# Kernel optimization log

Measured on AMD Instinct MI355X. Metric: run time of the kernel, lower is better.

## Reference

```python
import jax, jax.numpy as jnp
import numpy as np

SEQ_LEN = 256
INPUT_DIM = 1
HIDDEN = 1024
CLASSES = 10
BATCH = 256


def _uniform_param(key, shape, fan):
    # matches torch _parameter: uniform(-1/sqrt(y), 1/sqrt(y)), y = shape[1] if rank>1 else 1
    stdv = 1.0 / np.sqrt(fan)
    return jax.random.uniform(key, shape, jnp.float32, -stdv, stdv)


def setup_inputs() -> dict:
    key = jax.random.key(0)
    k0, k1, k2, k3, k4, k5 = jax.random.split(key, 6)
    x = jax.random.normal(k0, (BATCH, SEQ_LEN), jnp.float32)
    return {
        "x": x,
        "W_hx": _uniform_param(k1, (INPUT_DIM, HIDDEN), HIDDEN),
        "W_hh": _uniform_param(k2, (HIDDEN, HIDDEN), HIDDEN),
        "W_ph": _uniform_param(k3, (HIDDEN, CLASSES), CLASSES),
        "b_h": _uniform_param(k4, (HIDDEN,), 1),
        "b_p": _uniform_param(k5, (CLASSES,), 1),
    }


def reference(x, W_hx, W_hh, W_ph, b_h, b_p):
    # With INPUT_DIM == 1, x[:, t:t+1] is just column t; build [seq, batch, 1] for scan.
    xs = jnp.swapaxes(x, 0, 1)[:, :, None]  # [S, B, 1]
    h0 = jnp.zeros((x.shape[0], HIDDEN), x.dtype)

    def step(h_prev, x_t):
        h_t = jnp.tanh(x_t @ W_hx + h_prev @ W_hh + b_h)  # [B, H]
        return h_t, None

    h_last, _ = jax.lax.scan(step, h0, xs)
    # Original computes p_t each step but only returns the last; compute only the last.
    return h_last @ W_ph + b_p  # [B, C]
```

## Files before the change

### kernel.cpp

```cpp
#include <hip/hip_runtime.h>
#include <stdint.h>

#define SEQ   256
#define BATCH 256
#define HID   1024
#define NCLS  10

#define NWG     128
#define THREADS 512
#define PLANEB  (32 * 16 * 64 * 16)

typedef __attribute__((ext_vector_type(8))) short bf16x8;
typedef __attribute__((ext_vector_type(4))) float f32x4;
typedef __attribute__((ext_vector_type(4))) unsigned int u32x4;

__device__ __forceinline__ unsigned short f2bf(float f) {
  unsigned u = __builtin_bit_cast(unsigned, f);
  u = (u + 0x7FFFu + ((u >> 16) & 1u)) >> 16;
  return (unsigned short)u;
}
__device__ __forceinline__ float bf2f(unsigned short h) {
  unsigned u = ((unsigned)h) << 16;
  return __builtin_bit_cast(float, u);
}
__device__ __forceinline__ float fast_tanh(float x) {
  float ax = __builtin_fabsf(x);
  float e = __expf(2.0f * ax);
  float t = 1.0f - 2.0f / (e + 1.0f);
  return __builtin_copysignf(t, x);
}
__device__ __forceinline__ unsigned tag_of(unsigned t) {
  return ((t >> 1) & 1u) ^ 1u;
}

__global__ __launch_bounds__(THREADS, 2) void rnn_asmpoll(
    const float* __restrict__ x, const float* __restrict__ Whx,
    const float* __restrict__ Whh, const float* __restrict__ Wph,
    const float* __restrict__ bh, const float* __restrict__ bp,
    float* __restrict__ out, unsigned char* __restrict__ ws)
{
  __shared__ f32x4 red[8][7][64];
  __shared__ unsigned long long pkbuf[8][64];

  const int tid  = threadIdx.x;
  const int lane = tid & 63;
  const int wv   = tid >> 6;
  const int l15  = lane & 15;
  const int q    = lane >> 4;

  const int gb = blockIdx.x >> 4;
  const int s  = blockIdx.x & 15;

  unsigned char* p0 = ws;
  unsigned char* p1 = ws + PLANEB;

  bf16x8 whi[4][4], wlo[4][4];
#pragma unroll
  for (int i = 0; i < 4; ++i) {
    const int ks = wv * 4 + i;
#pragma unroll
    for (int rt = 0; rt < 4; ++rt) {
      const int n = s * 64 + rt * 16 + l15;
#pragma unroll
      for (int j = 0; j < 8; ++j) {
        int k = ks * 32 + 4 * q + (j & 3) + 16 * (j >> 2);
        float w = Whh[(size_t)k * HID + n];
        unsigned short hi = f2bf(w);
        whi[i][rt][j] = (short)hi;
        wlo[i][rt][j] = (short)f2bf(w - bf2f(hi));
      }
    }
  }

  const int rt_o = wv >> 1, bt_o = wv & 1;
  const int b_own = gb * 32 + bt_o * 16 + l15;
  const float* xrow = x + (size_t)b_own * SEQ;
  const float4 whx4 = *(const float4*)(Whx + s * 64 + rt_o * 16 + q * 4);
  const float4 bh4  = *(const float4*)(bh  + s * 64 + rt_o * 16 + q * 4);
  const size_t soff = ((size_t)((s * 2 + (wv >> 2)) * 16 + gb * 2 + (wv & 1)) * 64 + lane) * 16;
  volatile u32x4* st0 = (volatile u32x4*)(p0 + soff);
  volatile u32x4* st1 = (volatile u32x4*)(p1 + soff);

  const size_t oA0 = ((size_t)((wv * 4 + 0) * 16 + gb * 2) * 64 + lane) * 16;
  const size_t oA1 = ((size_t)((wv * 4 + 1) * 16 + gb * 2) * 64 + lane) * 16;
  const size_t oA2 = ((size_t)((wv * 4 + 2) * 16 + gb * 2) * 64 + lane) * 16;
  const size_t oA3 = ((size_t)((wv * 4 + 3) * 16 + gb * 2) * 64 + lane) * 16;

  for (int t = 0; t < SEQ; ++t) {
    const unsigned tauW = tag_of((unsigned)t);
    const float xb = xrow[t];

    f32x4 acc[4][2];
#pragma unroll
    for (int rt = 0; rt < 4; ++rt)
#pragma unroll
      for (int bt = 0; bt < 2; ++bt) acc[rt][bt] = (f32x4){0.f, 0.f, 0.f, 0.f};

    if (t > 0) {
      const unsigned tauR = tag_of((unsigned)(t - 1));
      const unsigned char* rp = (t & 1) ? p0 : p1;
      const unsigned char* b0 = rp + oA0;
      const unsigned char* b1 = rp + oA1;
      const unsigned char* b2 = rp + oA2;
      const unsigned char* b3 = rp + oA3;
      u32x4 f0, f1, f2, f3, f4, f5, f6, f7;

      for (;;) {
        unsigned s0, s1, s2, s3, s4, s5, s6, s7;
        asm volatile(
          "global_load_dword %0, %8, off sc0 sc1\n\t"
          "global_load_dword %1, %8, off offset:1024 sc0 sc1\n\t"
          "global_load_dword %2, %9, off sc0 sc1\n\t"
          "global_load_dword %3, %9, off offset:1024 sc0 sc1\n\t"
          "global_load_dword %4, %10, off sc0 sc1\n\t"
          "global_load_dword %5, %10, off offset:1024 sc0 sc1\n\t"
          "global_load_dword %6, %11, off sc0 sc1\n\t"
          "global_load_dword %7, %11, off offset:1024 sc0 sc1\n\t"
          "s_waitcnt vmcnt(0)"
          : "=&v"(s0), "=&v"(s1), "=&v"(s2), "=&v"(s3),
            "=&v"(s4), "=&v"(s5), "=&v"(s6), "=&v"(s7)
          : "v"(b0), "v"(b1), "v"(b2), "v"(b3)
          : "memory");
        __builtin_amdgcn_sched_barrier(0);
        unsigned bad = ((s0 ^ tauR) | (s1 ^ tauR) | (s2 ^ tauR) | (s3 ^ tauR) |
                        (s4 ^ tauR) | (s5 ^ tauR) | (s6 ^ tauR) | (s7 ^ tauR)) & 1u;
        if (!__all((int)(bad == 0))) { __builtin_amdgcn_s_sleep(1); continue; }

        asm volatile(
          "global_load_dwordx4 %0, %8, off sc0 sc1\n\t"
          "global_load_dwordx4 %1, %8, off offset:1024 sc0 sc1\n\t"
          "global_load_dwordx4 %2, %9, off sc0 sc1\n\t"
          "global_load_dwordx4 %3, %9, off offset:1024 sc0 sc1\n\t"
          "global_load_dwordx4 %4, %10, off sc0 sc1\n\t"
          "global_load_dwordx4 %5, %10, off offset:1024 sc0 sc1\n\t"
          "global_load_dwordx4 %6, %11, off sc0 sc1\n\t"
          "global_load_dwordx4 %7, %11, off offset:1024 sc0 sc1\n\t"
          "s_waitcnt vmcnt(0)"
          : "=&v"(f0), "=&v"(f1), "=&v"(f2), "=&v"(f3),
            "=&v"(f4), "=&v"(f5), "=&v"(f6), "=&v"(f7)
          : "v"(b0), "v"(b1), "v"(b2), "v"(b3)
          : "memory");
        __builtin_amdgcn_sched_barrier(0);
        unsigned vb = ((f0[0] ^ tauR) | (f0[1] ^ tauR) | (f0[2] ^ tauR) | (f0[3] ^ tauR) |
                       (f1[0] ^ tauR) | (f1[1] ^ tauR) | (f1[2] ^ tauR) | (f1[3] ^ tauR) |
                       (f2[0] ^ tauR) | (f2[1] ^ tauR) | (f2[2] ^ tauR) | (f2[3] ^ tauR) |
                       (f3[0] ^ tauR) | (f3[1] ^ tauR) | (f3[2] ^ tauR) | (f3[3] ^ tauR) |
                       (f4[0] ^ tauR) | (f4[1] ^ tauR) | (f4[2] ^ tauR) | (f4[3] ^ tauR) |
                       (f5[0] ^ tauR) | (f5[1] ^ tauR) | (f5[2] ^ tauR) | (f5[3] ^ tauR) |
                       (f6[0] ^ tauR) | (f6[1] ^ tauR) | (f6[2] ^ tauR) | (f6[3] ^ tauR) |
                       (f7[0] ^ tauR) | (f7[1] ^ tauR) | (f7[2] ^ tauR) | (f7[3] ^ tauR)) & 1u;
        if (__all((int)(vb == 0))) break;
        __builtin_amdgcn_s_sleep(1);
      }

#define MSTEP(F, I, BT)                                                        \
      { bf16x8 a_ = __builtin_bit_cast(bf16x8, F);                             \
        acc[0][BT] = __builtin_amdgcn_mfma_f32_16x16x32_bf16(whi[I][0], a_, acc[0][BT], 0, 0, 0); \
        acc[0][BT] = __builtin_amdgcn_mfma_f32_16x16x32_bf16(wlo[I][0], a_, acc[0][BT], 0, 0, 0); \
        acc[1][BT] = __builtin_amdgcn_mfma_f32_16x16x32_bf16(whi[I][1], a_, acc[1][BT], 0, 0, 0); \
        acc[1][BT] = __builtin_amdgcn_mfma_f32_16x16x32_bf16(wlo[I][1], a_, acc[1][BT], 0, 0, 0); \
        acc[2][BT] = __builtin_amdgcn_mfma_f32_16x16x32_bf16(whi[I][2], a_, acc[2][BT], 0, 0, 0); \
        acc[2][BT] = __builtin_amdgcn_mfma_f32_16x16x32_bf16(wlo[I][2], a_, acc[2][BT], 0, 0, 0); \
        acc[3][BT] = __builtin_amdgcn_mfma_f32_16x16x32_bf16(whi[I][3], a_, acc[3][BT], 0, 0, 0); \
        acc[3][BT] = __builtin_amdgcn_mfma_f32_16x16x32_bf16(wlo[I][3], a_, acc[3][BT], 0, 0, 0); }
      MSTEP(f0, 0, 0) MSTEP(f1, 0, 1) MSTEP(f2, 1, 0) MSTEP(f3, 1, 1)
      MSTEP(f4, 2, 0) MSTEP(f5, 2, 1) MSTEP(f6, 3, 0) MSTEP(f7, 3, 1)
#undef MSTEP
    }

#pragma unroll
    for (int T = 0; T < 8; ++T)
      if (T != wv)
        red[T][(wv > T) ? (wv - 1) : wv][lane] = acc[T >> 1][T & 1];
    __syncthreads();

    f32x4 ssum = acc[rt_o][bt_o];
#pragma unroll
    for (int pr = 0; pr < 7; ++pr) ssum += red[wv][pr][lane];

    const float v0 = fast_tanh(ssum[0] + xb * whx4.x + bh4.x);
    const float v1 = fast_tanh(ssum[1] + xb * whx4.y + bh4.y);
    const float v2 = fast_tanh(ssum[2] + xb * whx4.z + bh4.z);
    const float v3 = fast_tanh(ssum[3] + xb * whx4.w + bh4.w);
    unsigned w0 = ((unsigned)f2bf(v0) | ((unsigned)f2bf(v1) << 16));
    unsigned w1 = ((unsigned)f2bf(v2) | ((unsigned)f2bf(v3) << 16));
    w0 = (w0 & ~1u) | tauW;
    w1 = (w1 & ~1u) | tauW;
    unsigned long long pk = (unsigned long long)w0 | ((unsigned long long)w1 << 32);
    pkbuf[wv][lane] = pk;
    __syncthreads();

    if (!(wv & 2)) {
      unsigned long long pk2 = pkbuf[wv | 2][lane];
      u32x4 st;
      st[0] = (unsigned)pk;  st[1] = (unsigned)(pk >> 32);
      st[2] = (unsigned)pk2; st[3] = (unsigned)(pk2 >> 32);
      if (t & 1) *st1 = st; else *st0 = st;
    }
  }

  if (s != 0) return;
  {
    const unsigned tauF = tag_of(255u);
    u32x4 hf[4][2];
    for (;;) {
#pragma unroll
      for (int i = 0; i < 4; ++i)
#pragma unroll
        for (int bt = 0; bt < 2; ++bt)
          hf[i][bt] = *(const volatile u32x4*)
              (p1 + ((size_t)((wv * 4 + i) * 16 + gb * 2 + bt) * 64 + lane) * 16);
      unsigned bad = 0;
#pragma unroll
      for (int i = 0; i < 4; ++i)
#pragma unroll
        for (int bt = 0; bt < 2; ++bt)
#pragma unroll
          for (int w = 0; w < 4; ++w) bad |= (hf[i][bt][w] ^ tauF) & 1u;
      if (__all((int)(bad == 0))) break;
      __builtin_amdgcn_s_sleep(2);
    }

    float pr0[NCLS], pr1[NCLS];
#pragma unroll
    for (int c = 0; c < NCLS; ++c) { pr0[c] = 0.f; pr1[c] = 0.f; }
#pragma unroll
    for (int i = 0; i < 4; ++i) {
      const int ks = wv * 4 + i;
#pragma unroll
      for (int bt = 0; bt < 2; ++bt) {
#pragma unroll
        for (int w = 0; w < 4; ++w) {
          unsigned word = hf[i][bt][w];
#pragma unroll
          for (int h2 = 0; h2 < 2; ++h2) {
            int j = 2 * w + h2;
            int k = ks * 32 + 4 * q + (j & 3) + 16 * (j >> 2);
            float hv = bf2f((unsigned short)(h2 ? (word >> 16) : (word & 0xffffu)));
            const float* wrow = Wph + (size_t)k * NCLS;
#pragma unroll
            for (int c = 0; c < NCLS; ++c) {
              if (bt == 0) pr0[c] += hv * wrow[c];
              else         pr1[c] += hv * wrow[c];
            }
          }
        }
      }
    }
#pragma unroll
    for (int c = 0; c < NCLS; ++c) {
      pr0[c] += __shfl_xor(pr0[c], 16, 64); pr0[c] += __shfl_xor(pr0[c], 32, 64);
      pr1[c] += __shfl_xor(pr1[c], 16, 64); pr1[c] += __shfl_xor(pr1[c], 32, 64);
    }
    float* projl = (float*)&red[0][0][0];
    if (q == 0) {
#pragma unroll
      for (int c = 0; c < NCLS; ++c) {
        projl[((wv * 2 + 0) * 16 + l15) * NCLS + c] = pr0[c];
        projl[((wv * 2 + 1) * 16 + l15) * NCLS + c] = pr1[c];
      }
    }
    __syncthreads();
    if (tid < 32 * NCLS) {
      int bl = tid / NCLS, c = tid - bl * NCLS;
      float sum = bp[c];
#pragma unroll
      for (int w = 0; w < 8; ++w)
        sum += projl[((w * 2 + (bl >> 4)) * 16 + (bl & 15)) * NCLS + c];
      out[(size_t)(gb * 32 + bl) * NCLS + c] = sum;
    }
  }
}

extern "C" void kernel_launch(void* const* d_in, const int* in_sizes, int n_in,
                              void* d_out, int out_size, void* d_ws, size_t ws_size,
                              hipStream_t stream) {
  const float* x   = (const float*)d_in[0];
  const float* Whx = (const float*)d_in[1];
  const float* Whh = (const float*)d_in[2];
  const float* Wph = (const float*)d_in[3];
  const float* bh  = (const float*)d_in[4];
  const float* bp  = (const float*)d_in[5];

  hipLaunchKernelGGL(rnn_asmpoll, dim3(NWG), dim3(THREADS), 0, stream,
                     x, Whx, Whh, Wph, bh, bp,
                     (float*)d_out, (unsigned char*)d_ws);
}
```

Measured before the change: 1.498 ms.

## Use one barrier per step with double-buffered LDS reduction and drop tag pre-poll

```diff
diff --git a/kernel.cpp b/kernel.cpp
--- a/kernel.cpp
+++ b/kernel.cpp
@@ -33,14 +33,13 @@
   return ((t >> 1) & 1u) ^ 1u;
 }
 
-__global__ __launch_bounds__(THREADS, 2) void rnn_asmpoll(
+__global__ __launch_bounds__(THREADS, 1) void rnn_onebar(
     const float* __restrict__ x, const float* __restrict__ Whx,
     const float* __restrict__ Whh, const float* __restrict__ Wph,
     const float* __restrict__ bh, const float* __restrict__ bp,
     float* __restrict__ out, unsigned char* __restrict__ ws)
 {
-  __shared__ f32x4 red[8][7][64];
-  __shared__ unsigned long long pkbuf[8][64];
+  __shared__ f32x4 red[2][4][2][7][64];
 
   const int tid  = threadIdx.x;
   const int lane = tid & 63;
@@ -72,12 +71,15 @@
     }
   }
 
-  const int rt_o = wv >> 1, bt_o = wv & 1;
-  const int b_own = gb * 32 + bt_o * 16 + l15;
+  const int u_o  = wv >> 1, bt_oo = wv & 1;
+  const int b_own = gb * 32 + bt_oo * 16 + l15;
   const float* xrow = x + (size_t)b_own * SEQ;
-  const float4 whx4 = *(const float4*)(Whx + s * 64 + rt_o * 16 + q * 4);
-  const float4 bh4  = *(const float4*)(bh  + s * 64 + rt_o * 16 + q * 4);
-  const size_t soff = ((size_t)((s * 2 + (wv >> 2)) * 16 + gb * 2 + (wv & 1)) * 64 + lane) * 16;
+  float4 whxA, whxB, bhA, bhB;
+  whxA = *(const float4*)(Whx + s * 64 + (2 * u_o) * 16 + q * 4);
+  whxB = *(const float4*)(Whx + s * 64 + (2 * u_o + 1) * 16 + q * 4);
+  bhA  = *(const float4*)(bh  + s * 64 + (2 * u_o) * 16 + q * 4);
+  bhB  = *(const float4*)(bh  + s * 64 + (2 * u_o + 1) * 16 + q * 4);
+  const size_t soff = ((size_t)((s * 2 + u_o) * 16 + gb * 2 + bt_oo) * 64 + lane) * 16;
   volatile u32x4* st0 = (volatile u32x4*)(p0 + soff);
   volatile u32x4* st1 = (volatile u32x4*)(p1 + soff);
 
@@ -88,7 +90,7 @@
 
   for (int t = 0; t < SEQ; ++t) {
     const unsigned tauW = tag_of((unsigned)t);
-    const float xb = xrow[t];
+    const int buf = t & 1;
 
     f32x4 acc[4][2];
 #pragma unroll
@@ -106,26 +108,6 @@
       u32x4 f0, f1, f2, f3, f4, f5, f6, f7;
 
       for (;;) {
-        unsigned s0, s1, s2, s3, s4, s5, s6, s7;
-        asm volatile(
-          "global_load_dword %0, %8, off sc0 sc1\n\t"
-          "global_load_dword %1, %8, off offset:1024 sc0 sc1\n\t"
-          "global_load_dword %2, %9, off sc0 sc1\n\t"
-          "global_load_dword %3, %9, off offset:1024 sc0 sc1\n\t"
-          "global_load_dword %4, %10, off sc0 sc1\n\t"
-          "global_load_dword %5, %10, off offset:1024 sc0 sc1\n\t"
-          "global_load_dword %6, %11, off sc0 sc1\n\t"
-          "global_load_dword %7, %11, off offset:1024 sc0 sc1\n\t"
-          "s_waitcnt vmcnt(0)"
-          : "=&v"(s0), "=&v"(s1), "=&v"(s2), "=&v"(s3),
-            "=&v"(s4), "=&v"(s5), "=&v"(s6), "=&v"(s7)
-          : "v"(b0), "v"(b1), "v"(b2), "v"(b3)
-          : "memory");
-        __builtin_amdgcn_sched_barrier(0);
-        unsigned bad = ((s0 ^ tauR) | (s1 ^ tauR) | (s2 ^ tauR) | (s3 ^ tauR) |
-                        (s4 ^ tauR) | (s5 ^ tauR) | (s6 ^ tauR) | (s7 ^ tauR)) & 1u;
-        if (!__all((int)(bad == 0))) { __builtin_amdgcn_s_sleep(1); continue; }
-
         asm volatile(
           "global_load_dwordx4 %0, %8, off sc0 sc1\n\t"
           "global_load_dwordx4 %1, %8, off offset:1024 sc0 sc1\n\t"
@@ -169,33 +151,39 @@
     }
 
 #pragma unroll
-    for (int T = 0; T < 8; ++T)
-      if (T != wv)
-        red[T][(wv > T) ? (wv - 1) : wv][lane] = acc[T >> 1][T & 1];
+    for (int T = 0; T < 8; ++T) {
+      const int rt = T >> 1, bt = T & 1;
+      const int o = (rt & 2) | bt;
+      if (o != wv) {
+        const int slot = (wv > o) ? (wv - 1) : wv;
+        red[buf][rt][bt][slot][lane] = acc[rt][bt];
+      }
+    }
     __syncthreads();
 
-    f32x4 ssum = acc[rt_o][bt_o];
-#pragma unroll
-    for (int pr = 0; pr < 7; ++pr) ssum += red[wv][pr][lane];
-
-    const float v0 = fast_tanh(ssum[0] + xb * whx4.x + bh4.x);
-    const float v1 = fast_tanh(ssum[1] + xb * whx4.y + bh4.y);
-    const float v2 = fast_tanh(ssum[2] + xb * whx4.z + bh4.z);
-    const float v3 = fast_tanh(ssum[3] + xb * whx4.w + bh4.w);
-    unsigned w0 = ((unsigned)f2bf(v0) | ((unsigned)f2bf(v1) << 16));
-    unsigned w1 = ((unsigned)f2bf(v2) | ((unsigned)f2bf(v3) << 16));
-    w0 = (w0 & ~1u) | tauW;
-    w1 = (w1 & ~1u) | tauW;
-    unsigned long long pk = (unsigned long long)w0 | ((unsigned long long)w1 << 32);
-    pkbuf[wv][lane] = pk;
-    __syncthreads();
-
-    if (!(wv & 2)) {
-      unsigned long long pk2 = pkbuf[wv | 2][lane];
-      u32x4 st;
-      st[0] = (unsigned)pk;  st[1] = (unsigned)(pk >> 32);
-      st[2] = (unsigned)pk2; st[3] = (unsigned)(pk2 >> 32);
-      if (t & 1) *st1 = st; else *st0 = st;
+    if (wv < 4) {
+      f32x4 sA = acc[2 * u_o][bt_oo];
+      f32x4 sB = acc[2 * u_o + 1][bt_oo];
+#pragma unroll
+      for (int pr = 0; pr < 7; ++pr) {
+        sA += red[buf][2 * u_o][bt_oo][pr][lane];
+        sB += red[buf][2 * u_o + 1][bt_oo][pr][lane];
+      }
+      const float xb = xrow[t];
+      const float a0 = fast_tanh(sA[0] + xb * whxA.x + bhA.x);
+      const float a1 = fast_tanh(sA[1] + xb * whxA.y + bhA.y);
+      const float a2 = fast_tanh(sA[2] + xb * whxA.z + bhA.z);
+      const float a3 = fast_tanh(sA[3] + xb * whxA.w + bhA.w);
+      const float c0 = fast_tanh(sB[0] + xb * whxB.x + bhB.x);
+      const float c1 = fast_tanh(sB[1] + xb * whxB.y + bhB.y);
+      const float c2 = fast_tanh(sB[2] + xb * whxB.z + bhB.z);
+      const float c3 = fast_tanh(sB[3] + xb * whxB.w + bhB.w);
+      u32x4 stv;
+      stv[0] = (((unsigned)f2bf(a0) | ((unsigned)f2bf(a1) << 16)) & ~1u) | tauW;
+      stv[1] = (((unsigned)f2bf(a2) | ((unsigned)f2bf(a3) << 16)) & ~1u) | tauW;
+      stv[2] = (((unsigned)f2bf(c0) | ((unsigned)f2bf(c1) << 16)) & ~1u) | tauW;
+      stv[3] = (((unsigned)f2bf(c2) | ((unsigned)f2bf(c3) << 16)) & ~1u) | tauW;
+      if (t & 1) *st1 = stv; else *st0 = stv;
     }
   }
 
@@ -252,7 +240,7 @@
       pr0[c] += __shfl_xor(pr0[c], 16, 64); pr0[c] += __shfl_xor(pr0[c], 32, 64);
       pr1[c] += __shfl_xor(pr1[c], 16, 64); pr1[c] += __shfl_xor(pr1[c], 32, 64);
     }
-    float* projl = (float*)&red[0][0][0];
+    float* projl = (float*)&red[0][0][0][0][0];
     if (q == 0) {
 #pragma unroll
       for (int c = 0; c < NCLS; ++c) {
@@ -282,7 +270,7 @@
   const float* bh  = (const float*)d_in[4];
   const float* bp  = (const float*)d_in[5];
 
-  hipLaunchKernelGGL(rnn_asmpoll, dim3(NWG), dim3(THREADS), 0, stream,
+  hipLaunchKernelGGL(rnn_onebar, dim3(NWG), dim3(THREADS), 0, stream,
                      x, Whx, Whh, Wph, bh, bp,
                      (float*)d_out, (unsigned char*)d_ws);
 }
```

New measurement: 1.273 ms. -15.0%, faster.
